# Kernel tuning notes

Measured on AMD Instinct MI355X. Metric: run time of the kernel, lower is better.

The kernel has to match this reference:

```python
import jax, jax.numpy as jnp
import numpy as np

B = 16384          # batch
F = 26             # num sparse features
D = 13             # num dense features
V = 100000         # vocab per sparse feature
E = 16             # embedding size
HID = [400, 400, 400]
DNN_IN = F * E + D  # 429


def setup_inputs() -> dict:
    key = jax.random.key(0)
    ks = jax.random.split(key, 16)
    inp = {}
    inp["x_sparse"] = jax.random.randint(ks[0], (B, F), 0, V, dtype=jnp.int32)
    inp["x_dense"] = jax.random.uniform(ks[1], (B, D), dtype=jnp.float32)
    # embedding tables (stacked across features; all vocabs equal)
    inp["emb1"] = jax.random.normal(ks[2], (F, V, 1), dtype=jnp.float32) * 0.0001
    inp["emb2"] = jax.random.normal(ks[3], (F, V, E), dtype=jnp.float32) * 0.0001
    inp["w_dense"] = jax.random.normal(ks[4], (D, 1), dtype=jnp.float32) * 0.0001
    inp["bias"] = jnp.zeros((1,), dtype=jnp.float32)
    dims = [DNN_IN] + HID
    for i in range(3):
        inp[f"dnn_w{i}"] = jax.random.normal(ks[5 + i], (dims[i], dims[i + 1]), dtype=jnp.float32) * 0.02
        inp[f"dnn_b{i}"] = jnp.zeros((dims[i + 1],), dtype=jnp.float32)
    inp["final_w"] = jax.random.normal(ks[9], (HID[-1], 1), dtype=jnp.float32) * 0.02
    return inp


def reference(x_sparse, x_dense, emb1, emb2, w_dense, bias,
              dnn_w0, dnn_b0, dnn_w1, dnn_b1, dnn_w2, dnn_b2, final_w):
    f_idx = jnp.arange(F)[None, :]                      # [1, F]
    # FM linear: per-feature 1-d embedding lookup, summed over features
    e1 = emb1[f_idx, x_sparse, 0]                       # [B, F]
    linear_sparse = jnp.sum(e1, axis=-1, keepdims=True)  # [B, 1]
    linear_dense = x_dense @ w_dense                    # [B, 1]
    logit = linear_sparse + linear_dense
    # FM second order: square-of-sum minus sum-of-square
    fm = emb2[f_idx, x_sparse]                          # [B, F, E]
    s = jnp.sum(fm, axis=1)                             # [B, E]
    cross = 0.5 * jnp.sum(s * s - jnp.sum(fm * fm, axis=1), axis=-1, keepdims=True)  # [B, 1]
    logit = logit + cross
    # DNN
    h = jnp.concatenate([fm.reshape(x_sparse.shape[0], F * E), x_dense], axis=-1)  # [B, F*E+D]
    h = jax.nn.relu(h @ dnn_w0 + dnn_b0)
    h = jax.nn.relu(h @ dnn_w1 + dnn_b1)
    h = jax.nn.relu(h @ dnn_w2 + dnn_b2)
    logit = logit + h @ final_w                         # [B, 1]
    return jax.nn.sigmoid(logit + bias)
```

## Files before the change

kernel.cpp:

```cpp
#include <hip/hip_runtime.h>
#include <hip/hip_bf16.h>
#include <math.h>

#define BATCH 16384
#define NF 26
#define ND 13
#define VOC 100000
#define KP0 448
#define KP1 416
#define CS 80
#define NSL 5

typedef __bf16 bf16x8 __attribute__((ext_vector_type(8)));
typedef float f32x4 __attribute__((ext_vector_type(4)));
using bf16 = __hip_bfloat16;

__device__ __forceinline__ void gload_lds16(const void* g, void* l) {
  __builtin_amdgcn_global_load_lds(
      (const __attribute__((address_space(1))) void*)g,
      (__attribute__((address_space(3))) void*)l, 16, 0, 0);
}

__global__ void prep_kernel(const float* __restrict__ w0, const float* __restrict__ w1,
                            const float* __restrict__ w2, bf16* __restrict__ wt0,
                            bf16* __restrict__ wt1, bf16* __restrict__ wt2) {
  int bid = blockIdx.x, tid = threadIdx.x;
  const float* W; bf16* Wt; int K, KP, idx;
  if (bid < 728)       { W = w0; Wt = wt0; K = 429; KP = KP0; idx = bid * 256 + tid; }
  else if (bid < 1404) { W = w1; Wt = wt1; K = 400; KP = KP1; idx = (bid - 728) * 256 + tid; }
  else                 { W = w2; Wt = wt2; K = 400; KP = KP1; idx = (bid - 1404) * 256 + tid; }
  int k = idx % KP, n = idx / KP;
  float v = (k < K && n < 400) ? W[(size_t)k * 400 + n] : 0.f;
  Wt[idx] = __float2bfloat16(v);
}

__global__ __launch_bounds__(256) void gather_fm_kernel(
    const int* __restrict__ xs, const float* __restrict__ xd,
    const float* __restrict__ emb1, const float* __restrict__ emb2,
    const float* __restrict__ wd, const float* __restrict__ bias,
    bf16* __restrict__ h0, float* __restrict__ partial) {
  int gid = blockIdx.x * blockDim.x + threadIdx.x;
  int b = gid >> 6;
  int lane = threadIdx.x & 63;
  int fsub = lane >> 4;
  int e = lane & 15;
  float s_acc = 0.f, sq_acc = 0.f, lin = 0.f;
#pragma unroll
  for (int it = 0; it < 7; ++it) {
    int f = it * 4 + fsub;
    if (f < NF) {
      int idx = xs[b * NF + f];
      float v = emb2[((size_t)(f * VOC + idx)) * 16 + e];
      h0[(size_t)b * KP0 + f * 16 + e] = __float2bfloat16(v);
      s_acc += v;
      sq_acc += v * v;
      if (e == 0) lin += emb1[(size_t)f * VOC + idx];
    }
  }
  if (lane < 32) {
    float v = 0.f;
    if (lane < ND) { v = xd[b * ND + lane]; lin += v * wd[lane]; }
    h0[(size_t)b * KP0 + 416 + lane] = __float2bfloat16(v);
  }
  float s_tot = s_acc;
  s_tot += __shfl_xor(s_tot, 16);
  s_tot += __shfl_xor(s_tot, 32);
  float r0 = s_tot * s_tot;
  float r1 = sq_acc;
  float r2 = lin;
#pragma unroll
  for (int off = 1; off < 64; off <<= 1) {
    r0 += __shfl_xor(r0, off);
    r1 += __shfl_xor(r1, off);
    r2 += __shfl_xor(r2, off);
  }
  if (lane == 0) {
    float cross = 0.5f * (r0 * 0.25f - r1);
    partial[b] = bias[0] + r2 + cross;
  }
}

template <int NK, bool FINAL>
__global__ __launch_bounds__(256, 2) void gemm_kernel(
    const bf16* __restrict__ A, const bf16* __restrict__ Wt,
    const float* __restrict__ bias, bf16* __restrict__ outH,
    const float* __restrict__ fw, float* __restrict__ dotb) {
  constexpr int KP = NK * 32;
  extern __shared__ __align__(16) char smem[];
  const int b = blockIdx.x, tid = threadIdx.x;
  const int w = tid >> 6, lane = tid & 63, r = lane & 15, g = lane >> 4;
  const int lane8 = b & 7, hi = b >> 3;
  const int s = hi % NSL, mchunk = (hi / NSL) * 8 + lane8;
  const int row0 = mchunk * 128, col0 = s * CS;

  {
    const char* wbase = (const char*)(Wt + (size_t)col0 * KP);
    constexpr int T = NK * CS * 4;
    constexpr int FULL = T >> 8, REM = T & 255;
    for (int rd = 0; rd <= FULL; ++rd) {
      if (rd < FULL || tid < REM) {
        int c = rd * 256 + tid;
        int kk = c / (CS * 4), rm = c - kk * (CS * 4);
        int n = rm >> 2, j = rm & 3;
        int kc = j ^ ((n >> 1) & 3);
        gload_lds16(wbase + (size_t)n * (KP * 2) + kk * 64 + kc * 16,
                    smem + (rd * 256 + w * 64) * 16);
      }
    }
  }
  __syncthreads();

  const char* Ab = (const char*)(A + (size_t)(row0 + w * 32 + r) * KP) + g * 16;
  const size_t rtS = (size_t)16 * KP * 2;

  f32x4 acc[2][NSL];
#pragma unroll
  for (int rt = 0; rt < 2; ++rt)
#pragma unroll
    for (int ct = 0; ct < NSL; ++ct) acc[rt][ct] = (f32x4){0.f, 0.f, 0.f, 0.f};

  const int swz = ((g ^ ((r >> 1) & 3)) << 4);
  for (int k = 0; k < NK; ++k) {
    bf16x8 a0 = *(const bf16x8*)(Ab + k * 64);
    bf16x8 a1 = *(const bf16x8*)(Ab + k * 64 + rtS);
    const char* sb = smem + k * (CS * 64) + r * 64 + swz;
#pragma unroll
    for (int ct = 0; ct < NSL; ++ct) {
      bf16x8 bfr = *(const bf16x8*)(sb + ct * 1024);
      acc[0][ct] = __builtin_amdgcn_mfma_f32_16x16x32_bf16(a0, bfr, acc[0][ct], 0, 0, 0);
      acc[1][ct] = __builtin_amdgcn_mfma_f32_16x16x32_bf16(a1, bfr, acc[1][ct], 0, 0, 0);
    }
  }

  if (!FINAL) {
#pragma unroll
    for (int ct = 0; ct < NSL; ++ct) {
      int col = col0 + ct * 16 + r;
      float bv = bias[col];
#pragma unroll
      for (int rt = 0; rt < 2; ++rt)
#pragma unroll
        for (int q = 0; q < 4; ++q) {
          float v = fmaxf(acc[rt][ct][q] + bv, 0.f);
          outH[(size_t)(row0 + w * 32 + rt * 16 + g * 4 + q) * KP1 + col] =
              __float2bfloat16(v);
        }
    }
  } else {
    float pr[2][4] = {{0.f, 0.f, 0.f, 0.f}, {0.f, 0.f, 0.f, 0.f}};
#pragma unroll
    for (int ct = 0; ct < NSL; ++ct) {
      int col = col0 + ct * 16 + r;
      float bv = bias[col], fv = fw[col];
#pragma unroll
      for (int rt = 0; rt < 2; ++rt)
#pragma unroll
        for (int q = 0; q < 4; ++q)
          pr[rt][q] += fmaxf(acc[rt][ct][q] + bv, 0.f) * fv;
    }
#pragma unroll
    for (int rt = 0; rt < 2; ++rt)
#pragma unroll
      for (int q = 0; q < 4; ++q) {
        pr[rt][q] += __shfl_xor(pr[rt][q], 1);
        pr[rt][q] += __shfl_xor(pr[rt][q], 2);
        pr[rt][q] += __shfl_xor(pr[rt][q], 4);
        pr[rt][q] += __shfl_xor(pr[rt][q], 8);
      }
    if (r < 4) {
#pragma unroll
      for (int rt = 0; rt < 2; ++rt) {
        float v = (r == 0) ? pr[rt][0] : (r == 1) ? pr[rt][1]
                : (r == 2) ? pr[rt][2] : pr[rt][3];
        dotb[(size_t)s * BATCH + row0 + w * 32 + rt * 16 + g * 4 + r] = v;
      }
    }
  }
}

__global__ void finish_kernel(const float* __restrict__ partial,
                              const float* __restrict__ dotb,
                              float* __restrict__ out) {
  int i = blockIdx.x * 256 + threadIdx.x;
  if (i < BATCH) {
    float x = partial[i] + dotb[i] + dotb[BATCH + i] + dotb[2 * BATCH + i]
            + dotb[3 * BATCH + i] + dotb[4 * BATCH + i];
    out[i] = 1.f / (1.f + expf(-x));
  }
}

extern "C" void kernel_launch(void* const* d_in, const int* in_sizes, int n_in,
                              void* d_out, int out_size, void* d_ws, size_t ws_size,
                              hipStream_t stream) {
  const int* xs = (const int*)d_in[0];
  const float* xd = (const float*)d_in[1];
  const float* emb1 = (const float*)d_in[2];
  const float* emb2 = (const float*)d_in[3];
  const float* wd = (const float*)d_in[4];
  const float* bias = (const float*)d_in[5];
  const float* w0 = (const float*)d_in[6];
  const float* b0 = (const float*)d_in[7];
  const float* w1 = (const float*)d_in[8];
  const float* b1 = (const float*)d_in[9];
  const float* w2 = (const float*)d_in[10];
  const float* b2 = (const float*)d_in[11];
  const float* fw = (const float*)d_in[12];
  float* out = (float*)d_out;

  char* ws = (char*)d_ws;
  float* partial = (float*)(ws + 0);
  float* dotb    = (float*)(ws + 65536);
  bf16* wt0 = (bf16*)(ws + 393216);
  bf16* wt1 = (bf16*)(ws + 765952);
  bf16* wt2 = (bf16*)(ws + 1112064);
  bf16* h0  = (bf16*)(ws + 1458176);
  bf16* h1  = (bf16*)(ws + 16138240);
  bf16* h2  = (bf16*)(ws + 29769728);

  constexpr int LDS14 = 14 * CS * 64;
  constexpr int LDS13 = 13 * CS * 64;
  hipFuncSetAttribute((const void*)gemm_kernel<14, false>,
                      hipFuncAttributeMaxDynamicSharedMemorySize, LDS14);
  hipFuncSetAttribute((const void*)gemm_kernel<13, false>,
                      hipFuncAttributeMaxDynamicSharedMemorySize, LDS13);
  hipFuncSetAttribute((const void*)gemm_kernel<13, true>,
                      hipFuncAttributeMaxDynamicSharedMemorySize, LDS13);

  prep_kernel<<<2080, 256, 0, stream>>>(w0, w1, w2, wt0, wt1, wt2);
  gather_fm_kernel<<<BATCH / 4, 256, 0, stream>>>(xs, xd, emb1, emb2, wd, bias, h0, partial);

  gemm_kernel<14, false><<<640, 256, LDS14, stream>>>(h0, wt0, b0, h1, nullptr, nullptr);
  gemm_kernel<13, false><<<640, 256, LDS13, stream>>>(h1, wt1, b1, h2, nullptr, nullptr);
  gemm_kernel<13, true><<<640, 256, LDS13, stream>>>(h2, wt2, b2, nullptr, fw, dotb);

  finish_kernel<<<64, 256, 0, stream>>>(partial, dotb, out);
}
```

Before: 78.77 us.

## Fuse weight prep with gather and fold sigmoid finish into last GEMM

Merges the weight transpose/convert kernel and the embedding gather kernel into one launch, and removes the finish kernel. The last GEMM's blocks now use an atomic counter per row chunk, so the final block to arrive sums the partial dot products and applies the sigmoid. The gather is also restructured so each lane loads a float4 of an embedding row, with indices broadcast by shuffle, and writes packed bf16. This saves two launches and gives wider memory accesses, at the cost of atomics, fences and a counter reset done inside the fused kernel.

```diff
diff --git a/kernel.cpp b/kernel.cpp
--- a/kernel.cpp
+++ b/kernel.cpp
@@ -10,10 +10,12 @@
 #define KP1 416
 #define CS 80
 #define NSL 5
+#define NBP 2080
 
 typedef __bf16 bf16x8 __attribute__((ext_vector_type(8)));
 typedef float f32x4 __attribute__((ext_vector_type(4)));
 using bf16 = __hip_bfloat16;
+typedef unsigned short u16;
 
 __device__ __forceinline__ void gload_lds16(const void* g, void* l) {
   __builtin_amdgcn_global_load_lds(
@@ -21,70 +23,89 @@
       (__attribute__((address_space(3))) void*)l, 16, 0, 0);
 }
 
-__global__ void prep_kernel(const float* __restrict__ w0, const float* __restrict__ w1,
-                            const float* __restrict__ w2, bf16* __restrict__ wt0,
-                            bf16* __restrict__ wt1, bf16* __restrict__ wt2) {
-  int bid = blockIdx.x, tid = threadIdx.x;
-  const float* W; bf16* Wt; int K, KP, idx;
-  if (bid < 728)       { W = w0; Wt = wt0; K = 429; KP = KP0; idx = bid * 256 + tid; }
-  else if (bid < 1404) { W = w1; Wt = wt1; K = 400; KP = KP1; idx = (bid - 728) * 256 + tid; }
-  else                 { W = w2; Wt = wt2; K = 400; KP = KP1; idx = (bid - 1404) * 256 + tid; }
-  int k = idx % KP, n = idx / KP;
-  float v = (k < K && n < 400) ? W[(size_t)k * 400 + n] : 0.f;
-  Wt[idx] = __float2bfloat16(v);
-}
-
-__global__ __launch_bounds__(256) void gather_fm_kernel(
+__device__ __forceinline__ u16 f2bu(float v) {
+  union { __hip_bfloat16 b; u16 u; } cv;
+  cv.b = __float2bfloat16(v);
+  return cv.u;
+}
+
+__global__ __launch_bounds__(256) void prep_gather_kernel(
+    const float* __restrict__ w0, const float* __restrict__ w1,
+    const float* __restrict__ w2, bf16* __restrict__ wt0,
+    bf16* __restrict__ wt1, bf16* __restrict__ wt2,
     const int* __restrict__ xs, const float* __restrict__ xd,
     const float* __restrict__ emb1, const float* __restrict__ emb2,
-    const float* __restrict__ wd, const float* __restrict__ bias,
-    bf16* __restrict__ h0, float* __restrict__ partial) {
-  int gid = blockIdx.x * blockDim.x + threadIdx.x;
-  int b = gid >> 6;
-  int lane = threadIdx.x & 63;
-  int fsub = lane >> 4;
-  int e = lane & 15;
-  float s_acc = 0.f, sq_acc = 0.f, lin = 0.f;
-#pragma unroll
-  for (int it = 0; it < 7; ++it) {
-    int f = it * 4 + fsub;
+    const float* __restrict__ wd, const float* __restrict__ biasp,
+    bf16* __restrict__ h0, float* __restrict__ partial, int* __restrict__ cnt) {
+  const int bid = blockIdx.x, tid = threadIdx.x;
+  if (bid < NBP) {
+    const float* W; bf16* Wt; int K, KP, idx;
+    if (bid < 728)       { W = w0; Wt = wt0; K = 429; KP = KP0; idx = bid * 256 + tid; }
+    else if (bid < 1404) { W = w1; Wt = wt1; K = 400; KP = KP1; idx = (bid - 728) * 256 + tid; }
+    else                 { W = w2; Wt = wt2; K = 400; KP = KP1; idx = (bid - 1404) * 256 + tid; }
+    int k = idx % KP, n = idx / KP;
+    float v = (k < K && n < 400) ? W[(size_t)k * 400 + n] : 0.f;
+    Wt[idx] = __float2bfloat16(v);
+    return;
+  }
+  const int p = bid - NBP;
+  if (p == 0 && tid < 128) cnt[tid] = 0;
+  const int x8 = p & 7, qb = p >> 3;
+  const int gl = (qb >> 5) * 256 + x8 * 32 + (qb & 31);
+  const int w = tid >> 6, lane = tid & 63;
+  const int b = gl * 4 + w;
+  const int q = lane >> 2, sub = lane & 3;
+
+  int xsl = 0;
+  if (lane < NF) xsl = xs[b * NF + lane];
+  float lin = 0.f;
+  if (lane < NF) lin = emb1[(size_t)lane * VOC + xsl];
+  if (lane < ND) lin += xd[b * ND + lane] * wd[lane];
+
+  float4 sv = make_float4(0.f, 0.f, 0.f, 0.f);
+  float sq = 0.f;
+#pragma unroll
+  for (int i = 0; i < 2; ++i) {
+    int f = i * 16 + q;
     if (f < NF) {
-      int idx = xs[b * NF + f];
-      float v = emb2[((size_t)(f * VOC + idx)) * 16 + e];
-      h0[(size_t)b * KP0 + f * 16 + e] = __float2bfloat16(v);
-      s_acc += v;
-      sq_acc += v * v;
-      if (e == 0) lin += emb1[(size_t)f * VOC + idx];
+      int idx = __shfl(xsl, f);
+      float4 v = *((const float4*)(emb2 + ((size_t)f * VOC + idx) * 16) + sub);
+      sv.x += v.x; sv.y += v.y; sv.z += v.z; sv.w += v.w;
+      sq += v.x * v.x + v.y * v.y + v.z * v.z + v.w * v.w;
+      ushort4 st;
+      st.x = f2bu(v.x); st.y = f2bu(v.y); st.z = f2bu(v.z); st.w = f2bu(v.w);
+      *(ushort4*)(h0 + (size_t)b * KP0 + f * 16 + sub * 4) = st;
     }
   }
   if (lane < 32) {
-    float v = 0.f;
-    if (lane < ND) { v = xd[b * ND + lane]; lin += v * wd[lane]; }
+    float v = (lane < ND) ? xd[b * ND + lane] : 0.f;
     h0[(size_t)b * KP0 + 416 + lane] = __float2bfloat16(v);
   }
-  float s_tot = s_acc;
-  s_tot += __shfl_xor(s_tot, 16);
-  s_tot += __shfl_xor(s_tot, 32);
-  float r0 = s_tot * s_tot;
-  float r1 = sq_acc;
-  float r2 = lin;
+#pragma unroll
+  for (int off = 4; off < 64; off <<= 1) {
+    sv.x += __shfl_xor(sv.x, off);
+    sv.y += __shfl_xor(sv.y, off);
+    sv.z += __shfl_xor(sv.z, off);
+    sv.w += __shfl_xor(sv.w, off);
+  }
+  float t = sv.x * sv.x + sv.y * sv.y + sv.z * sv.z + sv.w * sv.w;
 #pragma unroll
   for (int off = 1; off < 64; off <<= 1) {
-    r0 += __shfl_xor(r0, off);
-    r1 += __shfl_xor(r1, off);
-    r2 += __shfl_xor(r2, off);
-  }
-  if (lane == 0) {
-    float cross = 0.5f * (r0 * 0.25f - r1);
-    partial[b] = bias[0] + r2 + cross;
-  }
+    t += __shfl_xor(t, off);
+    sq += __shfl_xor(sq, off);
+    lin += __shfl_xor(lin, off);
+  }
+  if (lane == 0)
+    partial[b] = biasp[0] + lin + 0.5f * (t * 0.0625f - sq);
 }
 
 template <int NK, bool FINAL>
 __global__ __launch_bounds__(256, 2) void gemm_kernel(
     const bf16* __restrict__ A, const bf16* __restrict__ Wt,
     const float* __restrict__ bias, bf16* __restrict__ outH,
-    const float* __restrict__ fw, float* __restrict__ dotb) {
+    const float* __restrict__ fw, float* __restrict__ dotb,
+    int* __restrict__ cnt, const float* __restrict__ partial,
+    float* __restrict__ outF) {
   constexpr int KP = NK * 32;
   extern __shared__ __align__(16) char smem[];
   const int b = blockIdx.x, tid = threadIdx.x;
@@ -175,17 +196,24 @@
         dotb[(size_t)s * BATCH + row0 + w * 32 + rt * 16 + g * 4 + r] = v;
       }
     }
-  }
-}
-
-__global__ void finish_kernel(const float* __restrict__ partial,
-                              const float* __restrict__ dotb,
-                              float* __restrict__ out) {
-  int i = blockIdx.x * 256 + threadIdx.x;
-  if (i < BATCH) {
-    float x = partial[i] + dotb[i] + dotb[BATCH + i] + dotb[2 * BATCH + i]
-            + dotb[3 * BATCH + i] + dotb[4 * BATCH + i];
-    out[i] = 1.f / (1.f + expf(-x));
+    __threadfence();
+    __syncthreads();
+    __shared__ int winflag;
+    if (tid == 0)
+      winflag = (atomicAdd(&cnt[mchunk], 1) == NSL - 1);
+    __syncthreads();
+    if (winflag) {
+      __threadfence();
+      if (tid < 128) {
+        int row = row0 + tid;
+        float xv = partial[row];
+#pragma unroll
+        for (int ss = 0; ss < NSL; ++ss)
+          xv += __hip_atomic_load(&dotb[(size_t)ss * BATCH + row],
+                                  __ATOMIC_RELAXED, __HIP_MEMORY_SCOPE_AGENT);
+        outF[row] = 1.f / (1.f + expf(-xv));
+      }
+    }
   }
 }
 
@@ -210,12 +238,13 @@
   char* ws = (char*)d_ws;
   float* partial = (float*)(ws + 0);
   float* dotb    = (float*)(ws + 65536);
-  bf16* wt0 = (bf16*)(ws + 393216);
-  bf16* wt1 = (bf16*)(ws + 765952);
-  bf16* wt2 = (bf16*)(ws + 1112064);
-  bf16* h0  = (bf16*)(ws + 1458176);
-  bf16* h1  = (bf16*)(ws + 16138240);
-  bf16* h2  = (bf16*)(ws + 29769728);
+  int*   cnt     = (int*)(ws + 393216);
+  bf16* wt0 = (bf16*)(ws + 409600);
+  bf16* wt1 = (bf16*)(ws + 782336);
+  bf16* wt2 = (bf16*)(ws + 1128448);
+  bf16* h0  = (bf16*)(ws + 1474560);
+  bf16* h1  = (bf16*)(ws + 16154624);
+  bf16* h2  = (bf16*)(ws + 29786112);
 
   constexpr int LDS14 = 14 * CS * 64;
   constexpr int LDS13 = 13 * CS * 64;
@@ -226,12 +255,13 @@
   hipFuncSetAttribute((const void*)gemm_kernel<13, true>,
                       hipFuncAttributeMaxDynamicSharedMemorySize, LDS13);
 
-  prep_kernel<<<2080, 256, 0, stream>>>(w0, w1, w2, wt0, wt1, wt2);
-  gather_fm_kernel<<<BATCH / 4, 256, 0, stream>>>(xs, xd, emb1, emb2, wd, bias, h0, partial);
-
-  gemm_kernel<14, false><<<640, 256, LDS14, stream>>>(h0, wt0, b0, h1, nullptr, nullptr);
-  gemm_kernel<13, false><<<640, 256, LDS13, stream>>>(h1, wt1, b1, h2, nullptr, nullptr);
-  gemm_kernel<13, true><<<640, 256, LDS13, stream>>>(h2, wt2, b2, nullptr, fw, dotb);
-
-  finish_kernel<<<64, 256, 0, stream>>>(partial, dotb, out);
-}
+  prep_gather_kernel<<<NBP + BATCH / 4, 256, 0, stream>>>(
+      w0, w1, w2, wt0, wt1, wt2, xs, xd, emb1, emb2, wd, bias, h0, partial, cnt);
+
+  gemm_kernel<14, false><<<640, 256, LDS14, stream>>>(
+      h0, wt0, b0, h1, nullptr, nullptr, nullptr, nullptr, nullptr);
+  gemm_kernel<13, false><<<640, 256, LDS13, stream>>>(
+      h1, wt1, b1, h2, nullptr, nullptr, nullptr, nullptr, nullptr);
+  gemm_kernel<13, true><<<640, 256, LDS13, stream>>>(
+      h2, wt2, b2, nullptr, fw, dotb, cnt, partial, out);
+}
```

Result: slower. 123.0 us (+56.1%).
